# Kernel tuning notes

Measured on AMD Instinct MI355X. Metric: run time of the kernel, lower is better.

Reference implementation:

```python
import jax, jax.numpy as jnp
import numpy as np

# Static config
B, C, H, W = 1, 4, 64, 64
DIM, NH = 512, 16
HD = DIM // NH
SCALE = HD ** -0.5
WC, WH, WW = 2, 8, 8            # 3D window size
N = WC * WH * WW                # tokens per window = 128
SC, SH, SW = 1, 4, 4            # shift = window // 2
NWC, NWH, NWW = C // WC, H // WH, W // WW
NWIN = NWC * NWH * NWW          # windows per sample
HID = 4 * DIM
NBLK = 2                        # [no-shift, shift] pair


def _rel_idx():
    coords = np.stack(np.meshgrid(np.arange(WC), np.arange(WH), np.arange(WW), indexing='ij')).reshape(3, -1)
    rel = coords[:, :, None] - coords[:, None, :]
    rel[0] += WC - 1; rel[1] += WH - 1; rel[2] += WW - 1
    idx = rel[0] * (2 * WH - 1) * (2 * WW - 1) + rel[1] * (2 * WW - 1) + rel[2]
    return jnp.asarray(idx)  # [N, N] into 675-entry table

REL_IDX = _rel_idx()


def _shift_mask():
    img = np.zeros((C, H, W), np.int32)
    cnt = 0
    for cs in (slice(0, -WC), slice(-WC, -SC), slice(-SC, None)):
        for hs in (slice(0, -WH), slice(-WH, -SH), slice(-SH, None)):
            for ws in (slice(0, -WW), slice(-WW, -SW), slice(-SW, None)):
                img[cs, hs, ws] = cnt; cnt += 1
    img = img.reshape(NWC, WC, NWH, WH, NWW, WW).transpose(0, 2, 4, 1, 3, 5).reshape(NWIN, N)
    diff = img[:, :, None] != img[:, None, :]
    return jnp.asarray(np.where(diff, -100.0, 0.0).astype(np.float32))  # [NWIN, N, N]

MASK = _shift_mask()


def _win_part(x):  # [B,C,H,W,D] -> [B*NWIN, N, D]
    x = x.reshape(B, NWC, WC, NWH, WH, NWW, WW, DIM)
    return x.transpose(0, 1, 3, 5, 2, 4, 6, 7).reshape(B * NWIN, N, DIM)


def _win_rev(x):  # [B*NWIN, N, D] -> [B,C,H,W,D]
    x = x.reshape(B, NWC, NWH, NWW, WC, WH, WW, DIM)
    return x.transpose(0, 1, 4, 2, 5, 3, 6, 7).reshape(B, C, H, W, DIM)


def _ln(x, g, b):
    m = x.mean(-1, keepdims=True)
    v = ((x - m) ** 2).mean(-1, keepdims=True)
    return (x - m) / jnp.sqrt(v + 1e-5) * g + b


def _forward(x, ln1_g, ln1_b, qkv_w, qkv_b, bias_tab, proj_w, proj_b,
             ln2_g, ln2_b, fc1_w, fc1_b, fc2_w, fc2_b):
    for i in range(NBLK):
        shifted = (i % 2 == 1)
        shortcut = x
        h = _ln(x, ln1_g[i], ln1_b[i]).reshape(B, C, H, W, DIM)
        if shifted:
            h = jnp.roll(h, (-SC, -SH, -SW), axis=(1, 2, 3))
        xw = _win_part(h)  # [B*NWIN, N, DIM]
        qkv = (xw @ qkv_w[i] + qkv_b[i]).reshape(-1, N, 3, NH, HD).transpose(2, 0, 3, 1, 4)
        q, k, v = qkv[0] * SCALE, qkv[1], qkv[2]       # [B*NWIN, NH, N, HD]
        bias = bias_tab[i][REL_IDX].transpose(2, 0, 1)  # [NH, N, N]
        attn = jnp.einsum('whnd,whmd->whnm', q, k) + bias[None]
        if shifted:
            attn = (attn.reshape(B, NWIN, NH, N, N) + MASK[None, :, None]).reshape(-1, NH, N, N)
        attn = jax.nn.softmax(attn, axis=-1)
        out = jnp.einsum('whnm,whmd->wnhd', attn, v).reshape(-1, N, DIM)
        out = out @ proj_w[i] + proj_b[i]
        h = _win_rev(out)
        if shifted:
            h = jnp.roll(h, (SC, SH, SW), axis=(1, 2, 3))
        x = shortcut + h.reshape(B, C * H * W, DIM)
        h2 = _ln(x, ln2_g[i], ln2_b[i])
        h2 = jax.nn.gelu(h2 @ fc1_w[i] + fc1_b[i], approximate=False) @ fc2_w[i] + fc2_b[i]
        x = x + h2
    return x


def setup_inputs() -> dict:
    key = jax.random.key(0)
    ks = jax.random.split(key, 8)
    s = 0.02
    return {
        'x': jax.random.normal(ks[0], (B, C * H * W, DIM), jnp.float32),
        'ln1_g': jnp.ones((NBLK, DIM), jnp.float32),
        'ln1_b': jnp.zeros((NBLK, DIM), jnp.float32),
        'qkv_w': jax.random.normal(ks[1], (NBLK, DIM, 3 * DIM), jnp.float32) * s,
        'qkv_b': jnp.zeros((NBLK, 3 * DIM), jnp.float32),
        'bias_tab': jax.random.normal(ks[2], (NBLK, (2 * WC - 1) * (2 * WH - 1) * (2 * WW - 1), NH), jnp.float32) * s,
        'proj_w': jax.random.normal(ks[3], (NBLK, DIM, DIM), jnp.float32) * s,
        'proj_b': jnp.zeros((NBLK, DIM), jnp.float32),
        'ln2_g': jnp.ones((NBLK, DIM), jnp.float32),
        'ln2_b': jnp.zeros((NBLK, DIM), jnp.float32),
        'fc1_w': jax.random.normal(ks[4], (NBLK, DIM, HID), jnp.float32) * s,
        'fc1_b': jnp.zeros((NBLK, HID), jnp.float32),
        'fc2_w': jax.random.normal(ks[5], (NBLK, HID, DIM), jnp.float32) * s,
        'fc2_b': jnp.zeros((NBLK, DIM), jnp.float32),
    }


def reference(x, ln1_g, ln1_b, qkv_w, qkv_b, bias_tab, proj_w, proj_b,
              ln2_g, ln2_b, fc1_w, fc1_b, fc2_w, fc2_b):
    return _forward(x, ln1_g, ln1_b, qkv_w, qkv_b, bias_tab, proj_w, proj_b,
                    ln2_g, ln2_b, fc1_w, fc1_b, fc2_w, fc2_b)
```

## Files before the change

kernel.cpp:

```cpp
#include <hip/hip_runtime.h>
#include <stdint.h>

#define DIM 512
#define NHD 16
#define HD 32
#define NTOK 16384

typedef unsigned short u16;
typedef __attribute__((ext_vector_type(8))) short short8;
typedef __attribute__((ext_vector_type(4))) float f32x4;

__device__ __forceinline__ float bflo(unsigned u){ union{unsigned i; float f;} c; c.i=u<<16; return c.f; }
__device__ __forceinline__ float bfhi(unsigned u){ union{unsigned i; float f;} c; c.i=u&0xffff0000u; return c.f; }
__device__ __forceinline__ u16 f2bf(float f){ union{float f; unsigned i;} c; c.f=f; unsigned r=(c.i + 0x7fffu + ((c.i>>16)&1u))>>16; return (u16)r; }

__device__ __forceinline__ int win_to_tok(int r, int shifted){
  int win = r >> 7, n = r & 127;
  int a = win >> 6, b = (win >> 3) & 7, c = win & 7;
  int ic = n >> 6, ih = (n >> 3) & 7, iw = n & 7;
  int gc = a*2 + ic, gh = b*8 + ih, gw = c*8 + iw;
  if (shifted){ gc = (gc + 1) & 3; gh = (gh + 4) & 63; gw = (gw + 4) & 63; }
  return (gc << 12) + (gh << 6) + gw;
}

__device__ __forceinline__ void gload16(const void* g, void* l){
  __builtin_amdgcn_global_load_lds(
    (const __attribute__((address_space(1))) unsigned int*)(unsigned long long)g,
    (__attribute__((address_space(3))) unsigned int*)(unsigned int)(unsigned long long)l,
    16, 0, 0);
}

__global__ __launch_bounds__(256)
void cvt_kernel(const float* __restrict__ in, u16* __restrict__ out)
{
  int i = blockIdx.x*256 + threadIdx.x;
  const float4* p = (const float4*)(in + (size_t)i*8);
  float4 a = p[0], b = p[1];
  union{u16 us[8]; uint4 u;} pk;
  pk.us[0]=f2bf(a.x); pk.us[1]=f2bf(a.y); pk.us[2]=f2bf(a.z); pk.us[3]=f2bf(a.w);
  pk.us[4]=f2bf(b.x); pk.us[5]=f2bf(b.y); pk.us[6]=f2bf(b.z); pk.us[7]=f2bf(b.w);
  ((uint4*)out)[i] = pk.u;
}

__global__ __launch_bounds__(256)
void transpose_kernel(const float* __restrict__ W, u16* __restrict__ Wt, int K, int N)
{
  __shared__ float t[32][33];
  size_t zoff = (size_t)blockIdx.z * K * N;
  int n0 = blockIdx.x*32, k0 = blockIdx.y*32;
  int tx = threadIdx.x & 31, ty = threadIdx.x >> 5;
  #pragma unroll
  for (int i=0;i<4;i++) t[ty + i*8][tx] = W[zoff + (size_t)(k0 + ty + i*8)*N + n0 + tx];
  __syncthreads();
  #pragma unroll
  for (int i=0;i<4;i++) Wt[zoff + (size_t)(n0 + ty + i*8)*K + k0 + tx] = f2bf(t[tx][ty + i*8]);
}

__global__ __launch_bounds__(256)
void ln_kernel(const u16* __restrict__ x, const float* __restrict__ g,
               const float* __restrict__ b, u16* __restrict__ out, int mode)
{
  int wave = threadIdx.x >> 6, lane = threadIdx.x & 63;
  int r = blockIdx.x * 4 + wave;
  int src = (mode < 0) ? r : win_to_tok(r, mode);
  uint4 u = ((const uint4*)(x + (size_t)src * DIM))[lane];
  unsigned w[4] = {u.x, u.y, u.z, u.w};
  float xv[8];
  #pragma unroll
  for (int j=0;j<4;j++){ xv[2*j] = bflo(w[j]); xv[2*j+1] = bfhi(w[j]); }
  float s = 0.f, sq = 0.f;
  #pragma unroll
  for (int j=0;j<8;j++){ s += xv[j]; sq += xv[j]*xv[j]; }
  #pragma unroll
  for (int o=32;o;o>>=1){ s += __shfl_xor(s,o); sq += __shfl_xor(sq,o); }
  float mean = s*(1.f/DIM);
  float var  = sq*(1.f/DIM) - mean*mean;
  float rstd = rsqrtf(var + 1e-5f);
  int c0 = lane*8;
  const float4* g4 = (const float4*)(g + c0);
  const float4* b4 = (const float4*)(b + c0);
  float4 ga = g4[0], gb = g4[1], ba = b4[0], bb = b4[1];
  float gg[8] = {ga.x,ga.y,ga.z,ga.w,gb.x,gb.y,gb.z,gb.w};
  float bv[8] = {ba.x,ba.y,ba.z,ba.w,bb.x,bb.y,bb.z,bb.w};
  union{u16 us[8]; uint4 u;} p;
  #pragma unroll
  for (int j=0;j<8;j++) p.us[j] = f2bf((xv[j]-mean)*rstd*gg[j] + bv[j]);
  ((uint4*)(out + (size_t)r*DIM))[lane] = p.u;
}

template<int EPI>
__global__ __launch_bounds__(256)
void gemm32r_kernel(const u16* __restrict__ X, const u16* __restrict__ Wt,
                    const float* __restrict__ bias, u16* __restrict__ obf,
                    u16* __restrict__ xbf, float* __restrict__ outf,
                    int M, int N, int K, int shifted)
{
  __shared__ u16 smem[24576];
  int tid = threadIdx.x, wave = tid>>6, lane = tid&63;
  int nwg = gridDim.x * gridDim.y;
  int bid = blockIdx.y * gridDim.x + blockIdx.x;
  int wg  = (bid & 7) * (nwg >> 3) + (bid >> 3);
  int n0 = (wg % gridDim.x) * 128;
  int m0 = (wg / gridDim.x) * 128;
  int wm = (wave>>1)*64, wn = (wave&1)*64;
  f32x4 acc[4][4] = {};

  int r_[2], c_[2];
  #pragma unroll
  for (int q=0;q<2;q++){
    int line = q*32 + (tid>>3), slot = tid&7;
    int u = slot ^ (line&7);
    r_[q] = line*2 + (u>>2); c_[q] = u&3;
  }

  auto stage = [&](int s, int kb){
    u16* Ad = smem + s*4096;
    u16* Bd = smem + 12288 + s*4096;
    #pragma unroll
    for (int q=0;q<2;q++){
      gload16(X + (size_t)(m0 + r_[q])*K + kb + c_[q]*8, (void*)(Ad + q*2048 + tid*8));
      gload16(Wt + (size_t)(n0 + r_[q])*K + kb + c_[q]*8, (void*)(Bd + q*2048 + tid*8));
    }
  };
  auto ldfrag = [&](const u16* base, int row0)->short8 {
    int r = row0 + (lane&15);
    int slot = (((r&1)<<2) + (lane>>4)) ^ ((r>>1)&7);
    return *(const short8*)((const char*)base + (r>>1)*128 + slot*16);
  };

  int nt = K >> 5;
  stage(0, 0); stage(1, 32);
  asm volatile("s_waitcnt vmcnt(4)" ::: "memory");
  __builtin_amdgcn_sched_barrier(0);
  __builtin_amdgcn_s_barrier();
  __builtin_amdgcn_sched_barrier(0);

  int s = 0;
  for (int t=0; t<nt; ++t){
    int s2 = s+2; if (s2>=3) s2-=3;
    if (t+2 < nt) stage(s2, (t+2)<<5);
    const u16* Ab = smem + s*4096;
    const u16* Bb = smem + 12288 + s*4096;
    short8 af[4], bfr[4];
    #pragma unroll
    for (int mi=0;mi<4;mi++) af[mi]  = ldfrag(Ab, wm + mi*16);
    #pragma unroll
    for (int nj=0;nj<4;nj++) bfr[nj] = ldfrag(Bb, wn + nj*16);
    __builtin_amdgcn_s_setprio(1);
    #pragma unroll
    for (int mi=0;mi<4;mi++)
      #pragma unroll
      for (int nj=0;nj<4;nj++)
        acc[mi][nj] = __builtin_amdgcn_mfma_f32_16x16x32_bf16(af[mi], bfr[nj], acc[mi][nj], 0,0,0);
    __builtin_amdgcn_s_setprio(0);
    asm volatile("s_waitcnt lgkmcnt(0)" ::: "memory");
    __builtin_amdgcn_sched_barrier(0);
    if (t+1 < nt){
      if (t+2 < nt) asm volatile("s_waitcnt vmcnt(4)" ::: "memory");
      else          asm volatile("s_waitcnt vmcnt(0)" ::: "memory");
      __builtin_amdgcn_sched_barrier(0);
    }
    __builtin_amdgcn_s_barrier();
    __builtin_amdgcn_sched_barrier(0);
    s = (s==2) ? 0 : s+1;
  }

  int lr = (lane>>4)*4, lc = lane&15;
  if (EPI==0 || EPI==2){
    u16* et = smem;
    #pragma unroll
    for (int mi=0;mi<4;mi++){
      #pragma unroll
      for (int nj=0;nj<4;nj++){
        int col = wn + nj*16 + lc;
        float bv = bias[n0 + col];
        #pragma unroll
        for (int rr=0;rr<4;rr++){
          int row = wm + mi*16 + lr + rr;
          float v = acc[mi][nj][rr] + bv;
          if (EPI==2){
            float u2 = v*(1.5957691216057308f + 0.0713548162726f*v*v);
            v = v * __builtin_amdgcn_rcpf(1.f + __expf(-u2));
          }
          *(u16*)((char*)et + ((row*256 + col*2) ^ (((row>>2)&3)<<5))) = f2bf(v);
        }
      }
    }
    __syncthreads();
    #pragma unroll
    for (int j=0;j<8;j++){
      int q = j*256 + tid;
      int row = q>>4, cc = q&15;
      uint4 d = *(const uint4*)((char*)et + ((row*256 + cc*16) ^ (((row>>2)&3)<<5)));
      *(uint4*)(obf + (size_t)(m0+row)*N + n0 + cc*8) = d;
    }
  } else {
    float* et = (float*)smem;
    #pragma unroll
    for (int half=0; half<2; ++half){
      __syncthreads();
      if ((wm>>6) == half){
        #pragma unroll
        for (int mi=0;mi<4;mi++){
          #pragma unroll
          for (int nj=0;nj<4;nj++){
            int col = wn + nj*16 + lc;
            float bv = bias[n0 + col];
            #pragma unroll
            for (int rr=0;rr<4;rr++){
              int row = (wm & 63) + mi*16 + lr + rr;
              *(float*)((char*)et + ((row*512 + col*4) ^ (((row>>2)&1)<<6))) = acc[mi][nj][rr] + bv;
            }
          }
        }
      }
      __syncthreads();
      #pragma unroll
      for (int j=0;j<4;j++){
        int q = j*256 + tid;
        int row = q>>4, c8 = q&15;
        int swz = ((row>>2)&1)<<6;
        float4 d0 = *(const float4*)((char*)et + ((row*512 + c8*32     ) ^ swz));
        float4 d1 = *(const float4*)((char*)et + ((row*512 + c8*32 + 16) ^ swz));
        int lrow = m0 + half*64 + row;
        int grow = (EPI==1) ? win_to_tok(lrow, shifted) : lrow;
        size_t gofs = (size_t)grow*DIM + n0 + c8*8;
        uint4 xv = *(const uint4*)(xbf + gofs);
        unsigned xw[4] = {xv.x, xv.y, xv.z, xv.w};
        float xs[8];
        #pragma unroll
        for (int k2=0;k2<4;k2++){ xs[2*k2] = bflo(xw[k2]); xs[2*k2+1] = bfhi(xw[k2]); }
        float ds[8] = {d0.x,d0.y,d0.z,d0.w,d1.x,d1.y,d1.z,d1.w};
        if (EPI==4){
          float4 o0 = {xs[0]+ds[0], xs[1]+ds[1], xs[2]+ds[2], xs[3]+ds[3]};
          float4 o1 = {xs[4]+ds[4], xs[5]+ds[5], xs[6]+ds[6], xs[7]+ds[7]};
          float4* op = (float4*)(outf + gofs);
          op[0] = o0; op[1] = o1;
        } else {
          union{u16 us[8]; uint4 u;} nw;
          #pragma unroll
          for (int k2=0;k2<8;k2++) nw.us[k2] = f2bf(xs[k2] + ds[k2]);
          *(uint4*)(xbf + gofs) = nw.u;
        }
      }
    }
  }
}

__global__ __launch_bounds__(256)
void bias_kernel(const float* __restrict__ btab, float* __restrict__ biasM)
{
  int gid = blockIdx.x*256 + threadIdx.x;
  int q = (gid >> 7) & 127, k = gid & 127, h = gid >> 14;
  int ic=q>>6, ih=(q>>3)&7, iw=q&7, jc=k>>6, jh=(k>>3)&7, jw=k&7;
  int idx = (ic-jc+1)*225 + (ih-jh+7)*15 + (iw-jw+7);
  biasM[gid] = btab[idx*16 + h];
}

__global__ __launch_bounds__(256)
void attn_kernel(const u16* __restrict__ qkv, const float* __restrict__ biasM,
                 u16* __restrict__ out, int shifted)
{
  __shared__ u16 Ks[128*32];
  __shared__ u16 VsT[32*128];
  __shared__ u16 Ps[4][32*128];
  __shared__ int rid[128];
  int win = blockIdx.x >> 4, h = blockIdx.x & 15;
  int tid = threadIdx.x, wave = tid>>6, lane = tid&63;
  size_t base = (size_t)win*128*1536 + (size_t)h*32;

  {
    int m = tid>>1, half = tid&1;
    const uint4* ks = (const uint4*)(qkv + base + (size_t)m*1536 + 512 + half*16);
    uint4 k0v = ks[0], k1v = ks[1];
    char* krow = (char*)Ks + m*64;
    int c0 = half*32, sw = (m&3)<<4;
    *(uint4*)(krow + ((c0     ) ^ sw)) = k0v;
    *(uint4*)(krow + ((c0 + 16) ^ sw)) = k1v;
    const uint4* vs = (const uint4*)(qkv + base + (size_t)m*1536 + 1024 + half*16);
    union{u16 us[16]; uint4 u[2];} vv; vv.u[0]=vs[0]; vv.u[1]=vs[1];
    #pragma unroll
    for (int j=0;j<16;j++){
      int d = half*16 + j;
      *(u16*)((char*)VsT + ((d*256 + m*2) ^ ((d&7)<<4))) = vv.us[j];
    }
  }
  if (shifted && tid < 128){
    int a=win>>6, b=(win>>3)&7, c=win&7;
    int gc=a*2+(tid>>6), gh=b*8+((tid>>3)&7), gw=c*8+(tid&7);
    int rc = (gc<2)?0:((gc<3)?1:2);
    int rh = (gh<56)?0:((gh<60)?1:2);
    int rw = (gw<56)?0:((gw<60)?1:2);
    rid[tid] = rc*9 + rh*3 + rw;
  }
  __syncthreads();

  int q0 = wave*32;
  short8 qf[2];
  #pragma unroll
  for (int mi=0;mi<2;mi++){
    int ql = 16*mi + (lane&15);
    qf[mi] = *(const short8*)(qkv + base + (size_t)(q0+ql)*1536 + (lane>>4)*8);
  }
  f32x4 s[2][8] = {};
  #pragma unroll
  for (int nj=0;nj<8;nj++){
    int row = (lane&15) + 16*nj;
    short8 kf = *(const short8*)((char*)Ks + row*64 + ((((lane>>4)<<4)) ^ ((row&3)<<4)));
    #pragma unroll
    for (int mi=0;mi<2;mi++)
      s[mi][nj] = __builtin_amdgcn_mfma_f32_16x16x32_bf16(qf[mi], kf, s[mi][nj], 0,0,0);
  }

  int rk[8];
  if (shifted){
    #pragma unroll
    for (int nj=0;nj<8;nj++) rk[nj] = rid[(lane&15) + 16*nj];
  }
  float invl[2][4];
  char* pbase = (char*)Ps[wave];
  #pragma unroll
  for (int mi=0;mi<2;mi++){
    #pragma unroll
    for (int r=0;r<4;r++){
      int ql = 16*mi + ((lane>>4)<<2) + r;
      int qw = q0 + ql;
      const float* bp = biasM + (((h<<7) + qw)<<7) + (lane&15);
      int rq = shifted ? rid[qw] : 0;
      float sv[8]; float mx = -1e30f;
      #pragma unroll
      for (int nj=0;nj<8;nj++){
        float v = s[mi][nj][r] * 0.17677669529663687f + bp[nj*16];
        if (shifted && rk[nj] != rq) v -= 100.f;
        sv[nj] = v; mx = fmaxf(mx, v);
      }
      #pragma unroll
      for (int o=1;o<16;o<<=1) mx = fmaxf(mx, __shfl_xor(mx, o));
      float sum = 0.f;
      #pragma unroll
      for (int nj=0;nj<8;nj++){ float p = __expf(sv[nj]-mx); sv[nj]=p; sum += p; }
      #pragma unroll
      for (int o=1;o<16;o<<=1) sum += __shfl_xor(sum, o);
      invl[mi][r] = 1.f/sum;
      char* prow = pbase + ql*256;
      int sw = (ql&7)<<4;
      #pragma unroll
      for (int nj=0;nj<8;nj++)
        *(u16*)(prow + ((((lane&15) + (nj<<4))<<1) ^ sw)) = f2bf(sv[nj]);
    }
  }

  f32x4 o2[2][2] = {};
  #pragma unroll
  for (int kk=0;kk<4;kk++){
    int coff = kk*64 + ((lane>>4)<<4);
    short8 pa[2], vb[2];
    #pragma unroll
    for (int mi=0;mi<2;mi++){
      int ql = 16*mi + (lane&15);
      pa[mi] = *(const short8*)(pbase + ql*256 + (coff ^ ((ql&7)<<4)));
    }
    #pragma unroll
    for (int nj=0;nj<2;nj++){
      int d = (lane&15) + 16*nj;
      vb[nj] = *(const short8*)((char*)VsT + d*256 + (coff ^ ((d&7)<<4)));
    }
    #pragma unroll
    for (int mi=0;mi<2;mi++)
      #pragma unroll
      for (int nj=0;nj<2;nj++)
        o2[mi][nj] = __builtin_amdgcn_mfma_f32_16x16x32_bf16(pa[mi], vb[nj], o2[mi][nj], 0,0,0);
  }

  #pragma unroll
  for (int mi=0;mi<2;mi++){
    #pragma unroll
    for (int nj=0;nj<2;nj++){
      #pragma unroll
      for (int r=0;r<4;r++){
        int ql = 16*mi + ((lane>>4)<<2) + r;
        int d  = (lane&15) + (nj<<4);
        out[(size_t)(win*128 + q0 + ql)*DIM + (h<<5) + d] = f2bf(o2[mi][nj][r] * invl[mi][r]);
      }
    }
  }
}

extern "C" void kernel_launch(void* const* d_in, const int* in_sizes, int n_in,
                              void* d_out, int out_size, void* d_ws, size_t ws_size,
                              hipStream_t stream)
{
  const float* x_in   = (const float*)d_in[0];
  const float* ln1_g  = (const float*)d_in[1];
  const float* ln1_b  = (const float*)d_in[2];
  const float* qkv_w  = (const float*)d_in[3];
  const float* qkv_b  = (const float*)d_in[4];
  const float* btab   = (const float*)d_in[5];
  const float* proj_w = (const float*)d_in[6];
  const float* proj_b = (const float*)d_in[7];
  const float* ln2_g  = (const float*)d_in[8];
  const float* ln2_b  = (const float*)d_in[9];
  const float* fc1_w  = (const float*)d_in[10];
  const float* fc1_b  = (const float*)d_in[11];
  const float* fc2_w  = (const float*)d_in[12];
  const float* fc2_b  = (const float*)d_in[13];

  char* ws = (char*)d_ws;
  size_t off = 0;
  auto alloc = [&](size_t bytes)->char*{ char* p = ws + off; off += (bytes + 255) & ~(size_t)255; return p; };
  u16* wT_qkv = (u16*)alloc((size_t)2*512*1536*2);
  u16* wT_proj= (u16*)alloc((size_t)2*512*512*2);
  u16* wT_fc1 = (u16*)alloc((size_t)2*2048*512*2);
  u16* wT_fc2 = (u16*)alloc((size_t)2*512*2048*2);
  u16* bufA   = (u16*)alloc((size_t)16384*2048*2);
  u16* bufQ   = (u16*)alloc((size_t)16384*1536*2);
  u16* bufB   = (u16*)alloc((size_t)16384*512*2);
  u16* xbf    = (u16*)alloc((size_t)16384*512*2);
  float* biasM= (float*)alloc((size_t)16*128*128*4);
  (void)ws_size; (void)in_sizes; (void)n_in; (void)out_size;

  float* xout = (float*)d_out;

  cvt_kernel<<<4096, 256, 0, stream>>>(x_in, xbf);

  transpose_kernel<<<dim3(1536/32, 512/32, 2), 256, 0, stream>>>(qkv_w, wT_qkv, 512, 1536);
  transpose_kernel<<<dim3( 512/32, 512/32, 2), 256, 0, stream>>>(proj_w, wT_proj, 512, 512);
  transpose_kernel<<<dim3(2048/32, 512/32, 2), 256, 0, stream>>>(fc1_w, wT_fc1, 512, 2048);
  transpose_kernel<<<dim3( 512/32,2048/32, 2), 256, 0, stream>>>(fc2_w, wT_fc2, 2048, 512);

  for (int i=0;i<2;i++){
    ln_kernel<<<4096, 256, 0, stream>>>(xbf, ln1_g+i*512, ln1_b+i*512, bufA, i);
    gemm32r_kernel<0><<<dim3(12,128), 256, 0, stream>>>(bufA, wT_qkv+(size_t)i*512*1536, qkv_b+i*1536, bufQ, nullptr, nullptr, NTOK,1536,512, 0);
    bias_kernel<<<1024, 256, 0, stream>>>(btab + (size_t)i*675*16, biasM);
    attn_kernel<<<2048, 256, 0, stream>>>(bufQ, biasM, bufB, i);
    gemm32r_kernel<1><<<dim3(4,128), 256, 0, stream>>>(bufB, wT_proj+(size_t)i*512*512, proj_b+i*512, nullptr, xbf, nullptr, NTOK,512,512, i);
    ln_kernel<<<4096, 256, 0, stream>>>(xbf, ln2_g+i*512, ln2_b+i*512, bufB, -1);
    gemm32r_kernel<2><<<dim3(16,128), 256, 0, stream>>>(bufB, wT_fc1+(size_t)i*2048*512, fc1_b+i*2048, bufA, nullptr, nullptr, NTOK,2048,512, 0);
    if (i==0)
      gemm32r_kernel<3><<<dim3(4,128), 256, 0, stream>>>(bufA, wT_fc2+(size_t)i*512*2048, fc2_b+i*512, nullptr, xbf, nullptr, NTOK,512,2048, 0);
    else
      gemm32r_kernel<4><<<dim3(4,128), 256, 0, stream>>>(bufA, wT_fc2+(size_t)i*512*2048, fc2_b+i*512, nullptr, xbf, xout, NTOK,512,2048, 0);
  }
}
```

Measured before the change: 424.6 us.

## Use per-wave private LDS staging in GEMM and fuse input cast into first LN

The GEMM now has each wave stage only its own 64-row A and B slices into a private double-buffered LDS region. This removes the workgroup-wide barrier from every k-step and issues the next prefetch right after the fragment reads complete. The cost is that A and B tiles shared across waves are loaded twice from global memory, and LDS use grows to 64KB, which may reduce occupancy. Separately, the fp32-to-bf16 input conversion is folded into the first LayerNorm kernel, which writes both the bf16 residual copy and the normalized output, removing one launch and one pass over memory.

```diff
diff --git a/kernel.cpp b/kernel.cpp
--- a/kernel.cpp
+++ b/kernel.cpp
@@ -31,18 +31,6 @@
 }
 
 __global__ __launch_bounds__(256)
-void cvt_kernel(const float* __restrict__ in, u16* __restrict__ out)
-{
-  int i = blockIdx.x*256 + threadIdx.x;
-  const float4* p = (const float4*)(in + (size_t)i*8);
-  float4 a = p[0], b = p[1];
-  union{u16 us[8]; uint4 u;} pk;
-  pk.us[0]=f2bf(a.x); pk.us[1]=f2bf(a.y); pk.us[2]=f2bf(a.z); pk.us[3]=f2bf(a.w);
-  pk.us[4]=f2bf(b.x); pk.us[5]=f2bf(b.y); pk.us[6]=f2bf(b.z); pk.us[7]=f2bf(b.w);
-  ((uint4*)out)[i] = pk.u;
-}
-
-__global__ __launch_bounds__(256)
 void transpose_kernel(const float* __restrict__ W, u16* __restrict__ Wt, int K, int N)
 {
   __shared__ float t[32][33];
@@ -57,17 +45,19 @@
 }
 
 __global__ __launch_bounds__(256)
-void ln_kernel(const u16* __restrict__ x, const float* __restrict__ g,
-               const float* __restrict__ b, u16* __restrict__ out, int mode)
+void ln_f32cvt_kernel(const float* __restrict__ x, const float* __restrict__ g,
+                      const float* __restrict__ b, u16* __restrict__ out, u16* __restrict__ xbf)
 {
   int wave = threadIdx.x >> 6, lane = threadIdx.x & 63;
   int r = blockIdx.x * 4 + wave;
-  int src = (mode < 0) ? r : win_to_tok(r, mode);
-  uint4 u = ((const uint4*)(x + (size_t)src * DIM))[lane];
-  unsigned w[4] = {u.x, u.y, u.z, u.w};
-  float xv[8];
-  #pragma unroll
-  for (int j=0;j<4;j++){ xv[2*j] = bflo(w[j]); xv[2*j+1] = bfhi(w[j]); }
+  int src = win_to_tok(r, 0);
+  const float4* xr = (const float4*)(x + (size_t)src * DIM);
+  float4 v0 = xr[lane*2], v1 = xr[lane*2+1];
+  float xv[8] = {v0.x,v0.y,v0.z,v0.w,v1.x,v1.y,v1.z,v1.w};
+  union{u16 us[8]; uint4 u;} raw;
+  #pragma unroll
+  for (int j=0;j<8;j++) raw.us[j] = f2bf(xv[j]);
+  ((uint4*)(xbf + (size_t)src*DIM))[lane] = raw.u;
   float s = 0.f, sq = 0.f;
   #pragma unroll
   for (int j=0;j<8;j++){ s += xv[j]; sq += xv[j]*xv[j]; }
@@ -88,14 +78,46 @@
   ((uint4*)(out + (size_t)r*DIM))[lane] = p.u;
 }
 
+__global__ __launch_bounds__(256)
+void ln_kernel(const u16* __restrict__ x, const float* __restrict__ g,
+               const float* __restrict__ b, u16* __restrict__ out, int mode)
+{
+  int wave = threadIdx.x >> 6, lane = threadIdx.x & 63;
+  int r = blockIdx.x * 4 + wave;
+  int src = (mode < 0) ? r : win_to_tok(r, mode);
+  uint4 u = ((const uint4*)(x + (size_t)src * DIM))[lane];
+  unsigned w[4] = {u.x, u.y, u.z, u.w};
+  float xv[8];
+  #pragma unroll
+  for (int j=0;j<4;j++){ xv[2*j] = bflo(w[j]); xv[2*j+1] = bfhi(w[j]); }
+  float s = 0.f, sq = 0.f;
+  #pragma unroll
+  for (int j=0;j<8;j++){ s += xv[j]; sq += xv[j]*xv[j]; }
+  #pragma unroll
+  for (int o=32;o;o>>=1){ s += __shfl_xor(s,o); sq += __shfl_xor(sq,o); }
+  float mean = s*(1.f/DIM);
+  float var  = sq*(1.f/DIM) - mean*mean;
+  float rstd = rsqrtf(var + 1e-5f);
+  int c0 = lane*8;
+  const float4* g4 = (const float4*)(g + c0);
+  const float4* b4 = (const float4*)(b + c0);
+  float4 ga = g4[0], gb = g4[1], ba = b4[0], bb = b4[1];
+  float gg[8] = {ga.x,ga.y,ga.z,ga.w,gb.x,gb.y,gb.z,gb.w};
+  float bv[8] = {ba.x,ba.y,ba.z,ba.w,bb.x,bb.y,bb.z,bb.w};
+  union{u16 us[8]; uint4 u;} p;
+  #pragma unroll
+  for (int j=0;j<8;j++) p.us[j] = f2bf((xv[j]-mean)*rstd*gg[j] + bv[j]);
+  ((uint4*)(out + (size_t)r*DIM))[lane] = p.u;
+}
+
 template<int EPI>
 __global__ __launch_bounds__(256)
-void gemm32r_kernel(const u16* __restrict__ X, const u16* __restrict__ Wt,
+void gemm32w_kernel(const u16* __restrict__ X, const u16* __restrict__ Wt,
                     const float* __restrict__ bias, u16* __restrict__ obf,
                     u16* __restrict__ xbf, float* __restrict__ outf,
                     int M, int N, int K, int shifted)
 {
-  __shared__ u16 smem[24576];
+  __shared__ u16 smem[32768];
   int tid = threadIdx.x, wave = tid>>6, lane = tid&63;
   int nwg = gridDim.x * gridDim.y;
   int bid = blockIdx.y * gridDim.x + blockIdx.x;
@@ -105,22 +127,23 @@
   int wm = (wave>>1)*64, wn = (wave&1)*64;
   f32x4 acc[4][4] = {};
 
-  int r_[2], c_[2];
-  #pragma unroll
-  for (int q=0;q<2;q++){
-    int line = q*32 + (tid>>3), slot = tid&7;
-    int u = slot ^ (line&7);
-    r_[q] = line*2 + (u>>2); c_[q] = u&3;
-  }
-
-  auto stage = [&](int s, int kb){
-    u16* Ad = smem + s*4096;
-    u16* Bd = smem + 12288 + s*4096;
-    #pragma unroll
-    for (int q=0;q<2;q++){
-      gload16(X + (size_t)(m0 + r_[q])*K + kb + c_[q]*8, (void*)(Ad + q*2048 + tid*8));
-      gload16(Wt + (size_t)(n0 + r_[q])*K + kb + c_[q]*8, (void*)(Bd + q*2048 + tid*8));
-    }
+  int u_ = (lane&7) ^ (lane>>3);
+  int rbase = ((lane>>3)<<1) + (u_>>2);
+  int cofs8 = (u_&3)*8;
+
+  const u16* Abase = X  + (size_t)(m0 + wm)*K;
+  const u16* Bbase = Wt + (size_t)(n0 + wn)*K;
+  u16* wreg = smem + wave*8192;
+
+  auto stage = [&](int c, int kb){
+    u16* Ad = wreg + c*4096;
+    u16* Bd = Ad + 2048;
+    #pragma unroll
+    for (int q=0;q<4;q++)
+      gload16(Abase + (size_t)(q*16 + rbase)*K + kb + cofs8, (void*)(Ad + q*512 + lane*8));
+    #pragma unroll
+    for (int q=0;q<4;q++)
+      gload16(Bbase + (size_t)(q*16 + rbase)*K + kb + cofs8, (void*)(Bd + q*512 + lane*8));
   };
   auto ldfrag = [&](const u16* base, int row0)->short8 {
     int r = row0 + (lane&15);
@@ -130,22 +153,21 @@
 
   int nt = K >> 5;
   stage(0, 0); stage(1, 32);
-  asm volatile("s_waitcnt vmcnt(4)" ::: "memory");
+  asm volatile("s_waitcnt vmcnt(8)" ::: "memory");
   __builtin_amdgcn_sched_barrier(0);
-  __builtin_amdgcn_s_barrier();
-  __builtin_amdgcn_sched_barrier(0);
-
-  int s = 0;
+
   for (int t=0; t<nt; ++t){
-    int s2 = s+2; if (s2>=3) s2-=3;
-    if (t+2 < nt) stage(s2, (t+2)<<5);
-    const u16* Ab = smem + s*4096;
-    const u16* Bb = smem + 12288 + s*4096;
+    int cur = t & 1;
+    const u16* Ab = wreg + cur*4096;
+    const u16* Bb = Ab + 2048;
     short8 af[4], bfr[4];
     #pragma unroll
-    for (int mi=0;mi<4;mi++) af[mi]  = ldfrag(Ab, wm + mi*16);
-    #pragma unroll
-    for (int nj=0;nj<4;nj++) bfr[nj] = ldfrag(Bb, wn + nj*16);
+    for (int mi=0;mi<4;mi++) af[mi]  = ldfrag(Ab, mi*16);
+    #pragma unroll
+    for (int nj=0;nj<4;nj++) bfr[nj] = ldfrag(Bb, nj*16);
+    asm volatile("s_waitcnt lgkmcnt(0)" ::: "memory");
+    __builtin_amdgcn_sched_barrier(0);
+    if (t+2 < nt) stage(cur, (t+2)<<5);
     __builtin_amdgcn_s_setprio(1);
     #pragma unroll
     for (int mi=0;mi<4;mi++)
@@ -153,18 +175,14 @@
       for (int nj=0;nj<4;nj++)
         acc[mi][nj] = __builtin_amdgcn_mfma_f32_16x16x32_bf16(af[mi], bfr[nj], acc[mi][nj], 0,0,0);
     __builtin_amdgcn_s_setprio(0);
-    asm volatile("s_waitcnt lgkmcnt(0)" ::: "memory");
-    __builtin_amdgcn_sched_barrier(0);
     if (t+1 < nt){
-      if (t+2 < nt) asm volatile("s_waitcnt vmcnt(4)" ::: "memory");
+      if (t+2 < nt) asm volatile("s_waitcnt vmcnt(8)" ::: "memory");
       else          asm volatile("s_waitcnt vmcnt(0)" ::: "memory");
       __builtin_amdgcn_sched_barrier(0);
     }
-    __builtin_amdgcn_s_barrier();
-    __builtin_amdgcn_sched_barrier(0);
-    s = (s==2) ? 0 : s+1;
-  }
-
+  }
+
+  __syncthreads();
   int lr = (lane>>4)*4, lc = lane&15;
   if (EPI==0 || EPI==2){
     u16* et = smem;
@@ -421,24 +439,25 @@
 
   float* xout = (float*)d_out;
 
-  cvt_kernel<<<4096, 256, 0, stream>>>(x_in, xbf);
-
   transpose_kernel<<<dim3(1536/32, 512/32, 2), 256, 0, stream>>>(qkv_w, wT_qkv, 512, 1536);
   transpose_kernel<<<dim3( 512/32, 512/32, 2), 256, 0, stream>>>(proj_w, wT_proj, 512, 512);
   transpose_kernel<<<dim3(2048/32, 512/32, 2), 256, 0, stream>>>(fc1_w, wT_fc1, 512, 2048);
   transpose_kernel<<<dim3( 512/32,2048/32, 2), 256, 0, stream>>>(fc2_w, wT_fc2, 2048, 512);
 
   for (int i=0;i<2;i++){
-    ln_kernel<<<4096, 256, 0, stream>>>(xbf, ln1_g+i*512, ln1_b+i*512, bufA, i);
-    gemm32r_kernel<0><<<dim3(12,128), 256, 0, stream>>>(bufA, wT_qkv+(size_t)i*512*1536, qkv_b+i*1536, bufQ, nullptr, nullptr, NTOK,1536,512, 0);
+    if (i==0)
+      ln_f32cvt_kernel<<<4096, 256, 0, stream>>>(x_in, ln1_g, ln1_b, bufA, xbf);
+    else
+      ln_kernel<<<4096, 256, 0, stream>>>(xbf, ln1_g+512, ln1_b+512, bufA, 1);
+    gemm32w_kernel<0><<<dim3(12,128), 256, 0, stream>>>(bufA, wT_qkv+(size_t)i*512*1536, qkv_b+i*1536, bufQ, nullptr, nullptr, NTOK,1536,512, 0);
     bias_kernel<<<1024, 256, 0, stream>>>(btab + (size_t)i*675*16, biasM);
     attn_kernel<<<2048, 256, 0, stream>>>(bufQ, biasM, bufB, i);
-    gemm32r_kernel<1><<<dim3(4,128), 256, 0, stream>>>(bufB, wT_proj+(size_t)i*512*512, proj_b+i*512, nullptr, xbf, nullptr, NTOK,512,512, i);
+    gemm32w_kernel<1><<<dim3(4,128), 256, 0, stream>>>(bufB, wT_proj+(size_t)i*512*512, proj_b+i*512, nullptr, xbf, nullptr, NTOK,512,512, i);
     ln_kernel<<<4096, 256, 0, stream>>>(xbf, ln2_g+i*512, ln2_b+i*512, bufB, -1);
-    gemm32r_kernel<2><<<dim3(16,128), 256, 0, stream>>>(bufB, wT_fc1+(size_t)i*2048*512, fc1_b+i*2048, bufA, nullptr, nullptr, NTOK,2048,512, 0);
+    gemm32w_kernel<2><<<dim3(16,128), 256, 0, stream>>>(bufB, wT_fc1+(size_t)i*2048*512, fc1_b+i*2048, bufA, nullptr, nullptr, NTOK,2048,512, 0);
     if (i==0)
-      gemm32r_kernel<3><<<dim3(4,128), 256, 0, stream>>>(bufA, wT_fc2+(size_t)i*512*2048, fc2_b+i*512, nullptr, xbf, nullptr, NTOK,512,2048, 0);
+      gemm32w_kernel<3><<<dim3(4,128), 256, 0, stream>>>(bufA, wT_fc2+(size_t)i*512*2048, fc2_b+i*512, nullptr, xbf, nullptr, NTOK,512,2048, 0);
     else
-      gemm32r_kernel<4><<<dim3(4,128), 256, 0, stream>>>(bufA, wT_fc2+(size_t)i*512*2048, fc2_b+i*512, nullptr, xbf, xout, NTOK,512,2048, 0);
-  }
-}
+      gemm32w_kernel<4><<<dim3(4,128), 256, 0, stream>>>(bufA, wT_fc2+(size_t)i*512*2048, fc2_b+i*512, nullptr, xbf, xout, NTOK,512,2048, 0);
+  }
+}
```

Result: slower. 492.2 us (+15.9%).

## Use 256x256 GEMM tiles for QKV and FC1, fuse input cast into first LayerNorm

Applied to the files above, without the earlier changes.

Adds a 512-thread GEMM kernel with 256x256 output tiles for the QKV and FC1 projections, replacing the 128x128-tile kernel there. Larger tiles give more operand reuse per LDS load but lower occupancy (one block per CU) and fewer workgroups (384 and 512). It also removes the separate fp32-to-bf16 conversion kernel by folding it into the first LayerNorm, which reads fp32 input and writes both the normalized windowed rows and the bf16 residual copy. That saves one pass over the input.

```diff
diff --git a/kernel.cpp b/kernel.cpp
--- a/kernel.cpp
+++ b/kernel.cpp
@@ -31,18 +31,6 @@
 }
 
 __global__ __launch_bounds__(256)
-void cvt_kernel(const float* __restrict__ in, u16* __restrict__ out)
-{
-  int i = blockIdx.x*256 + threadIdx.x;
-  const float4* p = (const float4*)(in + (size_t)i*8);
-  float4 a = p[0], b = p[1];
-  union{u16 us[8]; uint4 u;} pk;
-  pk.us[0]=f2bf(a.x); pk.us[1]=f2bf(a.y); pk.us[2]=f2bf(a.z); pk.us[3]=f2bf(a.w);
-  pk.us[4]=f2bf(b.x); pk.us[5]=f2bf(b.y); pk.us[6]=f2bf(b.z); pk.us[7]=f2bf(b.w);
-  ((uint4*)out)[i] = pk.u;
-}
-
-__global__ __launch_bounds__(256)
 void transpose_kernel(const float* __restrict__ W, u16* __restrict__ Wt, int K, int N)
 {
   __shared__ float t[32][33];
@@ -57,17 +45,19 @@
 }
 
 __global__ __launch_bounds__(256)
-void ln_kernel(const u16* __restrict__ x, const float* __restrict__ g,
-               const float* __restrict__ b, u16* __restrict__ out, int mode)
+void ln_f32cvt_kernel(const float* __restrict__ x, const float* __restrict__ g,
+                      const float* __restrict__ b, u16* __restrict__ out, u16* __restrict__ xbf)
 {
   int wave = threadIdx.x >> 6, lane = threadIdx.x & 63;
   int r = blockIdx.x * 4 + wave;
-  int src = (mode < 0) ? r : win_to_tok(r, mode);
-  uint4 u = ((const uint4*)(x + (size_t)src * DIM))[lane];
-  unsigned w[4] = {u.x, u.y, u.z, u.w};
-  float xv[8];
-  #pragma unroll
-  for (int j=0;j<4;j++){ xv[2*j] = bflo(w[j]); xv[2*j+1] = bfhi(w[j]); }
+  int src = win_to_tok(r, 0);
+  const float4* xr = (const float4*)(x + (size_t)src * DIM);
+  float4 v0 = xr[lane*2], v1 = xr[lane*2+1];
+  float xv[8] = {v0.x,v0.y,v0.z,v0.w,v1.x,v1.y,v1.z,v1.w};
+  union{u16 us[8]; uint4 u;} raw;
+  #pragma unroll
+  for (int j=0;j<8;j++) raw.us[j] = f2bf(xv[j]);
+  ((uint4*)(xbf + (size_t)src*DIM))[lane] = raw.u;
   float s = 0.f, sq = 0.f;
   #pragma unroll
   for (int j=0;j<8;j++){ s += xv[j]; sq += xv[j]*xv[j]; }
@@ -88,6 +78,157 @@
   ((uint4*)(out + (size_t)r*DIM))[lane] = p.u;
 }
 
+__global__ __launch_bounds__(256)
+void ln_kernel(const u16* __restrict__ x, const float* __restrict__ g,
+               const float* __restrict__ b, u16* __restrict__ out, int mode)
+{
+  int wave = threadIdx.x >> 6, lane = threadIdx.x & 63;
+  int r = blockIdx.x * 4 + wave;
+  int src = (mode < 0) ? r : win_to_tok(r, mode);
+  uint4 u = ((const uint4*)(x + (size_t)src * DIM))[lane];
+  unsigned w[4] = {u.x, u.y, u.z, u.w};
+  float xv[8];
+  #pragma unroll
+  for (int j=0;j<4;j++){ xv[2*j] = bflo(w[j]); xv[2*j+1] = bfhi(w[j]); }
+  float s = 0.f, sq = 0.f;
+  #pragma unroll
+  for (int j=0;j<8;j++){ s += xv[j]; sq += xv[j]*xv[j]; }
+  #pragma unroll
+  for (int o=32;o;o>>=1){ s += __shfl_xor(s,o); sq += __shfl_xor(sq,o); }
+  float mean = s*(1.f/DIM);
+  float var  = sq*(1.f/DIM) - mean*mean;
+  float rstd = rsqrtf(var + 1e-5f);
+  int c0 = lane*8;
+  const float4* g4 = (const float4*)(g + c0);
+  const float4* b4 = (const float4*)(b + c0);
+  float4 ga = g4[0], gb = g4[1], ba = b4[0], bb = b4[1];
+  float gg[8] = {ga.x,ga.y,ga.z,ga.w,gb.x,gb.y,gb.z,gb.w};
+  float bv[8] = {ba.x,ba.y,ba.z,ba.w,bb.x,bb.y,bb.z,bb.w};
+  union{u16 us[8]; uint4 u;} p;
+  #pragma unroll
+  for (int j=0;j<8;j++) p.us[j] = f2bf((xv[j]-mean)*rstd*gg[j] + bv[j]);
+  ((uint4*)(out + (size_t)r*DIM))[lane] = p.u;
+}
+
+template<int EPI>
+__global__ __launch_bounds__(512, 1)
+void gemm256r_kernel(const u16* __restrict__ X, const u16* __restrict__ Wt,
+                     const float* __restrict__ bias, u16* __restrict__ obf,
+                     int M, int N, int K)
+{
+  __shared__ u16 smem[49152];
+  int tid = threadIdx.x, wave = tid>>6, lane = tid&63;
+  int wr = wave>>2, wc = wave&3;
+  int nwg = gridDim.x * gridDim.y;
+  int bid = blockIdx.y * gridDim.x + blockIdx.x;
+  int wg  = (bid & 7) * (nwg >> 3) + (bid >> 3);
+  int n0 = (wg % gridDim.x) * 256;
+  int m0 = (wg / gridDim.x) * 256;
+  f32x4 acc[8][4] = {};
+
+  int reg_ = tid>>7, t7 = tid&127;
+  int rr_[2], cc_[2];
+  #pragma unroll
+  for (int q=0;q<2;q++){
+    int line = q*16 + (t7>>3), sl = tid&7;
+    int u = sl ^ (line&7);
+    rr_[q] = reg_*64 + line*2 + (u>>2);
+    cc_[q] = u&3;
+  }
+
+  auto stage = [&](int s, int kb){
+    u16* base = smem + s*16384;
+    #pragma unroll
+    for (int q=0;q<2;q++){
+      gload16(X  + (size_t)(m0 + rr_[q])*K + kb + cc_[q]*8, (void*)(base + reg_*2048 + q*1024 + t7*8));
+      gload16(Wt + (size_t)(n0 + rr_[q])*K + kb + cc_[q]*8, (void*)(base + 8192 + reg_*2048 + q*1024 + t7*8));
+    }
+  };
+  auto ldA = [&](int s, int mi)->short8{
+    int row = wr*128 + mi*16 + (lane&15);
+    int r = row&63;
+    int ch = ((((r&1)<<2) + (lane>>4)) ^ ((r>>1)&7));
+    return *(const short8*)((const char*)(smem + s*16384 + (row>>6)*2048) + (r>>1)*128 + ch*16);
+  };
+  auto ldB = [&](int s, int nj)->short8{
+    int row = wc*64 + nj*16 + (lane&15);
+    int r = row&63;
+    int ch = ((((r&1)<<2) + (lane>>4)) ^ ((r>>1)&7));
+    return *(const short8*)((const char*)(smem + s*16384 + 8192 + (row>>6)*2048) + (r>>1)*128 + ch*16);
+  };
+
+  int nt = K >> 5;
+  stage(0, 0); stage(1, 32);
+  asm volatile("s_waitcnt vmcnt(4)" ::: "memory");
+  __builtin_amdgcn_sched_barrier(0);
+  __builtin_amdgcn_s_barrier();
+  __builtin_amdgcn_sched_barrier(0);
+
+  int s = 0;
+  for (int t=0; t<nt; ++t){
+    int s2 = s+2; if (s2>=3) s2-=3;
+    if (t+2 < nt) stage(s2, (t+2)<<5);
+    short8 af[8], bfr[4];
+    #pragma unroll
+    for (int mi=0;mi<8;mi++) af[mi] = ldA(s, mi);
+    #pragma unroll
+    for (int nj=0;nj<4;nj++) bfr[nj] = ldB(s, nj);
+    __builtin_amdgcn_s_setprio(1);
+    #pragma unroll
+    for (int mi=0;mi<8;mi++)
+      #pragma unroll
+      for (int nj=0;nj<4;nj++)
+        acc[mi][nj] = __builtin_amdgcn_mfma_f32_16x16x32_bf16(af[mi], bfr[nj], acc[mi][nj], 0,0,0);
+    __builtin_amdgcn_s_setprio(0);
+    asm volatile("s_waitcnt lgkmcnt(0)" ::: "memory");
+    __builtin_amdgcn_sched_barrier(0);
+    if (t+1 < nt){
+      if (t+2 < nt) asm volatile("s_waitcnt vmcnt(4)" ::: "memory");
+      else          asm volatile("s_waitcnt vmcnt(0)" ::: "memory");
+      __builtin_amdgcn_sched_barrier(0);
+    }
+    __builtin_amdgcn_s_barrier();
+    __builtin_amdgcn_sched_barrier(0);
+    s = (s==2) ? 0 : s+1;
+  }
+
+  __syncthreads();
+  int lr = (lane>>4)*4, lc = lane&15;
+  u16* et = smem;
+  #pragma unroll
+  for (int half=0; half<2; ++half){
+    if (wr == half){
+      #pragma unroll
+      for (int mi=0;mi<8;mi++){
+        #pragma unroll
+        for (int nj=0;nj<4;nj++){
+          int col = wc*64 + nj*16 + lc;
+          float bv = bias[n0 + col];
+          #pragma unroll
+          for (int rx=0;rx<4;rx++){
+            int rowl = mi*16 + lr + rx;
+            float v = acc[mi][nj][rx] + bv;
+            if (EPI==2){
+              float u2 = v*(1.5957691216057308f + 0.0713548162726f*v*v);
+              v = v * __builtin_amdgcn_rcpf(1.f + __expf(-u2));
+            }
+            *(u16*)((char*)et + ((rowl*512 + col*2) ^ (((rowl>>2)&3)<<5))) = f2bf(v);
+          }
+        }
+      }
+    }
+    __syncthreads();
+    #pragma unroll
+    for (int j=0;j<8;j++){
+      int q = j*512 + tid;
+      int row = q>>5, cq = q&31;
+      uint4 d = *(const uint4*)((char*)et + ((row*512 + cq*16) ^ (((row>>2)&3)<<5)));
+      *(uint4*)(obf + (size_t)(m0 + half*128 + row)*N + n0 + cq*8) = d;
+    }
+    __syncthreads();
+  }
+}
+
 template<int EPI>
 __global__ __launch_bounds__(256)
 void gemm32r_kernel(const u16* __restrict__ X, const u16* __restrict__ Wt,
@@ -166,35 +307,7 @@
   }
 
   int lr = (lane>>4)*4, lc = lane&15;
-  if (EPI==0 || EPI==2){
-    u16* et = smem;
-    #pragma unroll
-    for (int mi=0;mi<4;mi++){
-      #pragma unroll
-      for (int nj=0;nj<4;nj++){
-        int col = wn + nj*16 + lc;
-        float bv = bias[n0 + col];
-        #pragma unroll
-        for (int rr=0;rr<4;rr++){
-          int row = wm + mi*16 + lr + rr;
-          float v = acc[mi][nj][rr] + bv;
-          if (EPI==2){
-            float u2 = v*(1.5957691216057308f + 0.0713548162726f*v*v);
-            v = v * __builtin_amdgcn_rcpf(1.f + __expf(-u2));
-          }
-          *(u16*)((char*)et + ((row*256 + col*2) ^ (((row>>2)&3)<<5))) = f2bf(v);
-        }
-      }
-    }
-    __syncthreads();
-    #pragma unroll
-    for (int j=0;j<8;j++){
-      int q = j*256 + tid;
-      int row = q>>4, cc = q&15;
-      uint4 d = *(const uint4*)((char*)et + ((row*256 + cc*16) ^ (((row>>2)&3)<<5)));
-      *(uint4*)(obf + (size_t)(m0+row)*N + n0 + cc*8) = d;
-    }
-  } else {
+  {
     float* et = (float*)smem;
     #pragma unroll
     for (int half=0; half<2; ++half){
@@ -207,9 +320,9 @@
             int col = wn + nj*16 + lc;
             float bv = bias[n0 + col];
             #pragma unroll
-            for (int rr=0;rr<4;rr++){
-              int row = (wm & 63) + mi*16 + lr + rr;
-              *(float*)((char*)et + ((row*512 + col*4) ^ (((row>>2)&1)<<6))) = acc[mi][nj][rr] + bv;
+            for (int rx=0;rx<4;rx++){
+              int row = (wm & 63) + mi*16 + lr + rx;
+              *(float*)((char*)et + ((row*512 + col*4) ^ (((row>>2)&1)<<6))) = acc[mi][nj][rx] + bv;
             }
           }
         }
@@ -421,21 +534,22 @@
 
   float* xout = (float*)d_out;
 
-  cvt_kernel<<<4096, 256, 0, stream>>>(x_in, xbf);
-
   transpose_kernel<<<dim3(1536/32, 512/32, 2), 256, 0, stream>>>(qkv_w, wT_qkv, 512, 1536);
   transpose_kernel<<<dim3( 512/32, 512/32, 2), 256, 0, stream>>>(proj_w, wT_proj, 512, 512);
   transpose_kernel<<<dim3(2048/32, 512/32, 2), 256, 0, stream>>>(fc1_w, wT_fc1, 512, 2048);
   transpose_kernel<<<dim3( 512/32,2048/32, 2), 256, 0, stream>>>(fc2_w, wT_fc2, 2048, 512);
 
   for (int i=0;i<2;i++){
-    ln_kernel<<<4096, 256, 0, stream>>>(xbf, ln1_g+i*512, ln1_b+i*512, bufA, i);
-    gemm32r_kernel<0><<<dim3(12,128), 256, 0, stream>>>(bufA, wT_qkv+(size_t)i*512*1536, qkv_b+i*1536, bufQ, nullptr, nullptr, NTOK,1536,512, 0);
+    if (i==0)
+      ln_f32cvt_kernel<<<4096, 256, 0, stream>>>(x_in, ln1_g, ln1_b, bufA, xbf);
+    else
+      ln_kernel<<<4096, 256, 0, stream>>>(xbf, ln1_g+512, ln1_b+512, bufA, 1);
+    gemm256r_kernel<0><<<dim3(6,64), 512, 0, stream>>>(bufA, wT_qkv+(size_t)i*512*1536, qkv_b+i*1536, bufQ, NTOK,1536,512);
     bias_kernel<<<1024, 256, 0, stream>>>(btab + (size_t)i*675*16, biasM);
     attn_kernel<<<2048, 256, 0, stream>>>(bufQ, biasM, bufB, i);
     gemm32r_kernel<1><<<dim3(4,128), 256, 0, stream>>>(bufB, wT_proj+(size_t)i*512*512, proj_b+i*512, nullptr, xbf, nullptr, NTOK,512,512, i);
     ln_kernel<<<4096, 256, 0, stream>>>(xbf, ln2_g+i*512, ln2_b+i*512, bufB, -1);
-    gemm32r_kernel<2><<<dim3(16,128), 256, 0, stream>>>(bufB, wT_fc1+(size_t)i*2048*512, fc1_b+i*2048, bufA, nullptr, nullptr, NTOK,2048,512, 0);
+    gemm256r_kernel<2><<<dim3(8,64), 512, 0, stream>>>(bufB, wT_fc1+(size_t)i*2048*512, fc1_b+i*2048, bufA, NTOK,2048,512);
     if (i==0)
       gemm32r_kernel<3><<<dim3(4,128), 256, 0, stream>>>(bufA, wT_fc2+(size_t)i*512*2048, fc2_b+i*512, nullptr, xbf, nullptr, NTOK,512,2048, 0);
     else
```

After: 455.2 us. 1.07x slower.

## Fuse input bf16 conversion into first LayerNorm and vectorize GEMM epilogue stores

Applied to the files above, without the earlier changes.

Drops the separate fp32-to-bf16 conversion kernel. The first LayerNorm now reads fp32 input directly and writes the bf16 residual copy as a side output, which saves one full pass over the activations and one launch. The MFMA operands are swapped so each lane holds four consecutive columns of one row. That lets the GEMM epilogues load bias as a float4 and write packed 8-byte or 16-byte LDS stores instead of scalar ones, with new swizzle patterns. The risk is new LDS bank-conflict behaviour, and any swizzle mismatch would give wrong results.

```diff
diff --git a/kernel.cpp b/kernel.cpp
--- a/kernel.cpp
+++ b/kernel.cpp
@@ -13,6 +13,7 @@
 __device__ __forceinline__ float bflo(unsigned u){ union{unsigned i; float f;} c; c.i=u<<16; return c.f; }
 __device__ __forceinline__ float bfhi(unsigned u){ union{unsigned i; float f;} c; c.i=u&0xffff0000u; return c.f; }
 __device__ __forceinline__ u16 f2bf(float f){ union{float f; unsigned i;} c; c.f=f; unsigned r=(c.i + 0x7fffu + ((c.i>>16)&1u))>>16; return (u16)r; }
+__device__ __forceinline__ unsigned pk2(float a, float b){ return (unsigned)f2bf(a) | ((unsigned)f2bf(b)<<16); }
 
 __device__ __forceinline__ int win_to_tok(int r, int shifted){
   int win = r >> 7, n = r & 127;
@@ -31,18 +32,6 @@
 }
 
 __global__ __launch_bounds__(256)
-void cvt_kernel(const float* __restrict__ in, u16* __restrict__ out)
-{
-  int i = blockIdx.x*256 + threadIdx.x;
-  const float4* p = (const float4*)(in + (size_t)i*8);
-  float4 a = p[0], b = p[1];
-  union{u16 us[8]; uint4 u;} pk;
-  pk.us[0]=f2bf(a.x); pk.us[1]=f2bf(a.y); pk.us[2]=f2bf(a.z); pk.us[3]=f2bf(a.w);
-  pk.us[4]=f2bf(b.x); pk.us[5]=f2bf(b.y); pk.us[6]=f2bf(b.z); pk.us[7]=f2bf(b.w);
-  ((uint4*)out)[i] = pk.u;
-}
-
-__global__ __launch_bounds__(256)
 void transpose_kernel(const float* __restrict__ W, u16* __restrict__ Wt, int K, int N)
 {
   __shared__ float t[32][33];
@@ -57,17 +46,19 @@
 }
 
 __global__ __launch_bounds__(256)
-void ln_kernel(const u16* __restrict__ x, const float* __restrict__ g,
-               const float* __restrict__ b, u16* __restrict__ out, int mode)
+void ln_f32cvt_kernel(const float* __restrict__ x, const float* __restrict__ g,
+                      const float* __restrict__ b, u16* __restrict__ out, u16* __restrict__ xbf)
 {
   int wave = threadIdx.x >> 6, lane = threadIdx.x & 63;
   int r = blockIdx.x * 4 + wave;
-  int src = (mode < 0) ? r : win_to_tok(r, mode);
-  uint4 u = ((const uint4*)(x + (size_t)src * DIM))[lane];
-  unsigned w[4] = {u.x, u.y, u.z, u.w};
-  float xv[8];
-  #pragma unroll
-  for (int j=0;j<4;j++){ xv[2*j] = bflo(w[j]); xv[2*j+1] = bfhi(w[j]); }
+  int src = win_to_tok(r, 0);
+  const float4* xr = (const float4*)(x + (size_t)src * DIM);
+  float4 v0 = xr[lane*2], v1 = xr[lane*2+1];
+  float xv[8] = {v0.x,v0.y,v0.z,v0.w,v1.x,v1.y,v1.z,v1.w};
+  union{u16 us[8]; uint4 u;} raw;
+  #pragma unroll
+  for (int j=0;j<8;j++) raw.us[j] = f2bf(xv[j]);
+  ((uint4*)(xbf + (size_t)src*DIM))[lane] = raw.u;
   float s = 0.f, sq = 0.f;
   #pragma unroll
   for (int j=0;j<8;j++){ s += xv[j]; sq += xv[j]*xv[j]; }
@@ -88,6 +79,38 @@
   ((uint4*)(out + (size_t)r*DIM))[lane] = p.u;
 }
 
+__global__ __launch_bounds__(256)
+void ln_kernel(const u16* __restrict__ x, const float* __restrict__ g,
+               const float* __restrict__ b, u16* __restrict__ out, int mode)
+{
+  int wave = threadIdx.x >> 6, lane = threadIdx.x & 63;
+  int r = blockIdx.x * 4 + wave;
+  int src = (mode < 0) ? r : win_to_tok(r, mode);
+  uint4 u = ((const uint4*)(x + (size_t)src * DIM))[lane];
+  unsigned w[4] = {u.x, u.y, u.z, u.w};
+  float xv[8];
+  #pragma unroll
+  for (int j=0;j<4;j++){ xv[2*j] = bflo(w[j]); xv[2*j+1] = bfhi(w[j]); }
+  float s = 0.f, sq = 0.f;
+  #pragma unroll
+  for (int j=0;j<8;j++){ s += xv[j]; sq += xv[j]*xv[j]; }
+  #pragma unroll
+  for (int o=32;o;o>>=1){ s += __shfl_xor(s,o); sq += __shfl_xor(sq,o); }
+  float mean = s*(1.f/DIM);
+  float var  = sq*(1.f/DIM) - mean*mean;
+  float rstd = rsqrtf(var + 1e-5f);
+  int c0 = lane*8;
+  const float4* g4 = (const float4*)(g + c0);
+  const float4* b4 = (const float4*)(b + c0);
+  float4 ga = g4[0], gb = g4[1], ba = b4[0], bb = b4[1];
+  float gg[8] = {ga.x,ga.y,ga.z,ga.w,gb.x,gb.y,gb.z,gb.w};
+  float bv[8] = {ba.x,ba.y,ba.z,ba.w,bb.x,bb.y,bb.z,bb.w};
+  union{u16 us[8]; uint4 u;} p;
+  #pragma unroll
+  for (int j=0;j<8;j++) p.us[j] = f2bf((xv[j]-mean)*rstd*gg[j] + bv[j]);
+  ((uint4*)(out + (size_t)r*DIM))[lane] = p.u;
+}
+
 template<int EPI>
 __global__ __launch_bounds__(256)
 void gemm32r_kernel(const u16* __restrict__ X, const u16* __restrict__ Wt,
@@ -151,7 +174,7 @@
     for (int mi=0;mi<4;mi++)
       #pragma unroll
       for (int nj=0;nj<4;nj++)
-        acc[mi][nj] = __builtin_amdgcn_mfma_f32_16x16x32_bf16(af[mi], bfr[nj], acc[mi][nj], 0,0,0);
+        acc[mi][nj] = __builtin_amdgcn_mfma_f32_16x16x32_bf16(bfr[nj], af[mi], acc[mi][nj], 0,0,0);
     __builtin_amdgcn_s_setprio(0);
     asm volatile("s_waitcnt lgkmcnt(0)" ::: "memory");
     __builtin_amdgcn_sched_barrier(0);
@@ -165,25 +188,30 @@
     s = (s==2) ? 0 : s+1;
   }
 
-  int lr = (lane>>4)*4, lc = lane&15;
   if (EPI==0 || EPI==2){
     u16* et = smem;
     #pragma unroll
     for (int mi=0;mi<4;mi++){
+      int row = wm + mi*16 + (lane&15);
+      int swz = ((row>>1)&7)<<4;
       #pragma unroll
       for (int nj=0;nj<4;nj++){
-        int col = wn + nj*16 + lc;
-        float bv = bias[n0 + col];
-        #pragma unroll
-        for (int rr=0;rr<4;rr++){
-          int row = wm + mi*16 + lr + rr;
-          float v = acc[mi][nj][rr] + bv;
-          if (EPI==2){
-            float u2 = v*(1.5957691216057308f + 0.0713548162726f*v*v);
-            v = v * __builtin_amdgcn_rcpf(1.f + __expf(-u2));
-          }
-          *(u16*)((char*)et + ((row*256 + col*2) ^ (((row>>2)&3)<<5))) = f2bf(v);
+        int col0 = wn + nj*16 + ((lane>>4)<<2);
+        float4 bv = *(const float4*)(bias + n0 + col0);
+        float v0 = acc[mi][nj][0] + bv.x, v1 = acc[mi][nj][1] + bv.y;
+        float v2 = acc[mi][nj][2] + bv.z, v3 = acc[mi][nj][3] + bv.w;
+        if (EPI==2){
+          float u0 = v0*(1.5957691216057308f + 0.0713548162726f*v0*v0);
+          float u1 = v1*(1.5957691216057308f + 0.0713548162726f*v1*v1);
+          float u2 = v2*(1.5957691216057308f + 0.0713548162726f*v2*v2);
+          float u3 = v3*(1.5957691216057308f + 0.0713548162726f*v3*v3);
+          v0 *= __builtin_amdgcn_rcpf(1.f + __expf(-u0));
+          v1 *= __builtin_amdgcn_rcpf(1.f + __expf(-u1));
+          v2 *= __builtin_amdgcn_rcpf(1.f + __expf(-u2));
+          v3 *= __builtin_amdgcn_rcpf(1.f + __expf(-u3));
         }
+        uint2 pkd = { pk2(v0,v1), pk2(v2,v3) };
+        *(uint2*)((char*)et + ((row*256 + col0*2) ^ swz)) = pkd;
       }
     }
     __syncthreads();
@@ -191,7 +219,7 @@
     for (int j=0;j<8;j++){
       int q = j*256 + tid;
       int row = q>>4, cc = q&15;
-      uint4 d = *(const uint4*)((char*)et + ((row*256 + cc*16) ^ (((row>>2)&3)<<5)));
+      uint4 d = *(const uint4*)((char*)et + ((row*256 + cc*16) ^ (((row>>1)&7)<<4)));
       *(uint4*)(obf + (size_t)(m0+row)*N + n0 + cc*8) = d;
     }
   } else {
@@ -202,15 +230,15 @@
       if ((wm>>6) == half){
         #pragma unroll
         for (int mi=0;mi<4;mi++){
+          int row = (wm & 63) + mi*16 + (lane&15);
+          int swz = (row&7)<<4;
           #pragma unroll
           for (int nj=0;nj<4;nj++){
-            int col = wn + nj*16 + lc;
-            float bv = bias[n0 + col];
-            #pragma unroll
-            for (int rr=0;rr<4;rr++){
-              int row = (wm & 63) + mi*16 + lr + rr;
-              *(float*)((char*)et + ((row*512 + col*4) ^ (((row>>2)&1)<<6))) = acc[mi][nj][rr] + bv;
-            }
+            int col0 = wn + nj*16 + ((lane>>4)<<2);
+            float4 bv = *(const float4*)(bias + n0 + col0);
+            float4 wv = { acc[mi][nj][0] + bv.x, acc[mi][nj][1] + bv.y,
+                          acc[mi][nj][2] + bv.z, acc[mi][nj][3] + bv.w };
+            *(float4*)((char*)et + ((row*512 + col0*4) ^ swz)) = wv;
           }
         }
       }
@@ -219,7 +247,7 @@
       for (int j=0;j<4;j++){
         int q = j*256 + tid;
         int row = q>>4, c8 = q&15;
-        int swz = ((row>>2)&1)<<6;
+        int swz = (row&7)<<4;
         float4 d0 = *(const float4*)((char*)et + ((row*512 + c8*32     ) ^ swz));
         float4 d1 = *(const float4*)((char*)et + ((row*512 + c8*32 + 16) ^ swz));
         int lrow = m0 + half*64 + row;
@@ -421,15 +449,16 @@
 
   float* xout = (float*)d_out;
 
-  cvt_kernel<<<4096, 256, 0, stream>>>(x_in, xbf);
-
   transpose_kernel<<<dim3(1536/32, 512/32, 2), 256, 0, stream>>>(qkv_w, wT_qkv, 512, 1536);
   transpose_kernel<<<dim3( 512/32, 512/32, 2), 256, 0, stream>>>(proj_w, wT_proj, 512, 512);
   transpose_kernel<<<dim3(2048/32, 512/32, 2), 256, 0, stream>>>(fc1_w, wT_fc1, 512, 2048);
   transpose_kernel<<<dim3( 512/32,2048/32, 2), 256, 0, stream>>>(fc2_w, wT_fc2, 2048, 512);
 
   for (int i=0;i<2;i++){
-    ln_kernel<<<4096, 256, 0, stream>>>(xbf, ln1_g+i*512, ln1_b+i*512, bufA, i);
+    if (i==0)
+      ln_f32cvt_kernel<<<4096, 256, 0, stream>>>(x_in, ln1_g, ln1_b, bufA, xbf);
+    else
+      ln_kernel<<<4096, 256, 0, stream>>>(xbf, ln1_g+512, ln1_b+512, bufA, 1);
     gemm32r_kernel<0><<<dim3(12,128), 256, 0, stream>>>(bufA, wT_qkv+(size_t)i*512*1536, qkv_b+i*1536, bufQ, nullptr, nullptr, NTOK,1536,512, 0);
     bias_kernel<<<1024, 256, 0, stream>>>(btab + (size_t)i*675*16, biasM);
     attn_kernel<<<2048, 256, 0, stream>>>(bufQ, biasM, bufB, i);
```

New measurement: 436.4 us. +2.8%, slower.
